# Optimization experiments

Measured on AMD Instinct MI355X. Metric: run time of the kernel, lower is better.

## Reference

```python
import jax, jax.numpy as jnp
import numpy as np

V, E, H, L, T, B, S = 50000, 256, 512, 2, 22, 64, 512
HH = H // 2
START, STOP = T - 2, T - 1  # START_TAG, STOP_TAG appended to tagset


def _lstm_cell(x, h, c, wih, whh, b):
    # PyTorch gate order: i, f, g, o
    g = x @ wih.T + h @ whh.T + b
    i, f, gg, o = jnp.split(g, 4, axis=-1)
    c2 = jax.nn.sigmoid(f) * c + jax.nn.sigmoid(i) * jnp.tanh(gg)
    h2 = jax.nn.sigmoid(o) * jnp.tanh(c2)
    return h2, c2


def _run_dir(xs, ms, h0, c0, wih, whh, b, reverse):
    # xs: [S,B,E], ms: [S,B] bool. Packed-sequence semantics: no state update
    # and zero (pad-value) output at padded steps.
    def step(carry, inp):
        h, c = carry
        xt, mt = inp
        h2, c2 = _lstm_cell(xt, h, c, wih, whh, b)
        m = mt[:, None]
        h = jnp.where(m, h2, h)
        c = jnp.where(m, c2, c)
        return (h, c), jnp.where(m, h, 0.0)
    _, outs = jax.lax.scan(step, (h0, c0), (xs, ms), reverse=reverse)
    return outs


def _forward_feats(sentence, lengths, emb, wih_f, whh_f, b_f, wih_b, whh_b, b_b,
                   h1_0, c1_0, wih_s, whh_s, b_s, h2_0, c2_0, W_tag, b_tag):
    Bq, Sq = sentence.shape
    x = emb[sentence]                                       # [B,S,E]
    ms = (jnp.arange(Sq)[None, :] < lengths[:, None]).T     # [S,B]
    xs = jnp.transpose(x, (1, 0, 2))                        # [S,B,E]
    bc = lambda p: jnp.broadcast_to(p, (Bq, p.shape[-1]))
    out_f = _run_dir(xs, ms, bc(h1_0[0]), bc(c1_0[0]), wih_f, whh_f, b_f, False)
    out_b = _run_dir(xs, ms, bc(h1_0[1]), bc(c1_0[1]), wih_b, whh_b, b_b, True)
    bi = jnp.concatenate([out_f, out_b], axis=-1)           # [S,B,H]

    h0 = jnp.broadcast_to(h2_0, (L, Bq, H))
    c0 = jnp.broadcast_to(c2_0, (L, Bq, H))

    def step(carry, xt):
        h, c = carry
        inp = xt
        hs, cs = [], []
        for l in range(L):  # small fixed layer count
            h2, c2 = _lstm_cell(inp, h[l], c[l], wih_s[l], whh_s[l], b_s[l])
            inp = h2
            hs.append(h2)
            cs.append(c2)
        return (jnp.stack(hs), jnp.stack(cs)), inp

    _, outs = jax.lax.scan(step, (h0, c0), bi)              # [S,B,H]
    feats = jnp.einsum('sbh,th->sbt', outs, W_tag) + b_tag  # [S,B,T]
    return feats, ms


def _viterbi(feats, ms, trans):
    # trans[i, j] = score of transitioning from tag j to tag i
    Tn = trans.shape[0]
    score = feats[0] + trans[:, START][None, :]             # [B,T]

    def vstep(score, inp):
        ft, mt = inp
        cand = score[:, None, :] + trans[None, :, :]        # [B, to, from]
        ns = jnp.max(cand, axis=2) + ft
        bp = jnp.argmax(cand, axis=2)
        m = mt[:, None]
        score = jnp.where(m, ns, score)
        bp = jnp.where(m, bp, jnp.arange(Tn)[None, :])      # identity at pad
        return score, bp

    score, bps = jax.lax.scan(vstep, score, (feats[1:], ms[1:]))
    terminal = score + trans[STOP][None, :]
    best_score = jnp.max(terminal, axis=1)                  # [B]
    best_tag = jnp.argmax(terminal, axis=1)                 # [B]

    def bt(tag, bp):
        nt = jnp.take_along_axis(bp, tag[:, None], axis=1)[:, 0]
        return nt, nt

    _, rest = jax.lax.scan(bt, best_tag, bps, reverse=True)  # [S-1,B]
    tags = jnp.concatenate([rest, best_tag[None, :]], axis=0).T  # [B,S]
    return best_score, tags


def setup_inputs() -> dict:
    key = jax.random.key(0)
    ks = iter(jax.random.split(key, 24))
    sc = 0.08
    n = lambda shape: jax.random.normal(next(ks), shape, dtype=jnp.float32) * sc
    return dict(
        sentence=jax.random.randint(next(ks), (B, S), 0, V),
        lengths=jax.random.randint(next(ks), (B,), 1, S + 1),
        emb=n((V, E)),
        wih_f=n((4 * HH, E)), whh_f=n((4 * HH, HH)), b_f=n((4 * HH,)),
        wih_b=n((4 * HH, E)), whh_b=n((4 * HH, HH)), b_b=n((4 * HH,)),
        h1_0=n((2, 1, HH)), c1_0=n((2, 1, HH)),
        wih_s=n((L, 4 * H, H)), whh_s=n((L, 4 * H, H)), b_s=n((L, 4 * H)),
        h2_0=n((L, 1, H)), c2_0=n((L, 1, H)),
        W_tag=n((T, H)), b_tag=n((T,)),
        trans=n((T, T)),
    )


def reference(sentence, lengths, emb, wih_f, whh_f, b_f, wih_b, whh_b, b_b,
              h1_0, c1_0, wih_s, whh_s, b_s, h2_0, c2_0, W_tag, b_tag, trans):
    feats, ms = _forward_feats(sentence, lengths, emb, wih_f, whh_f, b_f,
                               wih_b, whh_b, b_b, h1_0, c1_0,
                               wih_s, whh_s, b_s, h2_0, c2_0, W_tag, b_tag)
    score, tag_seq = _viterbi(feats, ms, trans)
    return score, tag_seq
```

## Files before the change

### kernel.cpp

```cpp
#include <hip/hip_runtime.h>
#include <cmath>


namespace {
constexpr int SS = 512;
constexpr int BB = 64;
constexpr int EE = 256;
constexpr int HHd = 256;
constexpr int HD = 512;
constexpr int NTAG = 22;
constexpr int TSTART = 20;
constexpr int TSTOP = 21;

constexpr size_t OFF_BI    = 0;
constexpr size_t OFF_H1H   = OFF_BI    + (size_t)SS * HD * BB;
constexpr size_t OFF_XT    = OFF_H1H   + (size_t)(SS + 1) * HD * BB;
constexpr size_t OFF_FEATS = OFF_XT    + (size_t)SS * EE * BB;
constexpr size_t OFF_H0R   = OFF_FEATS + (size_t)SS * NTAG * BB;
constexpr size_t OFF_HF    = OFF_H0R   + 2 * (size_t)HD * BB;
constexpr size_t OFF_HB    = OFF_HF    + 2 * (size_t)HHd * BB;
constexpr size_t OFF_BAR   = OFF_HB    + 2 * (size_t)HHd * BB;
constexpr int BAR_INTS = 1152;

constexpr size_t OFF_C0 = OFF_XT;
constexpr size_t OFF_C1 = OFF_XT + (size_t)HD * BB;
}

__device__ __forceinline__ int cidx(int k, int lane) {
  return ((k >> 2) << 8) + (lane << 2) + (k & 3);
}

__device__ __forceinline__ float4 cload4(const float4* p) {
  float4 r;
  asm volatile("global_load_dwordx4 %0, %1, off sc0 sc1" : "=v"(r) : "v"(p));
  return r;
}
__device__ __forceinline__ void vwait0() {
  asm volatile("s_waitcnt vmcnt(0)" ::: "memory");
}
__device__ __forceinline__ void cstore(float* p, float v) {
  __hip_atomic_store(p, v, __ATOMIC_RELAXED, __HIP_MEMORY_SCOPE_AGENT);
}

template <int NBLK>
__device__ __forceinline__ void gbarC(int* flags, int* release, int bid, int epoch) {
  __syncthreads();
  if (threadIdx.x == 0) {
    __hip_atomic_store(flags + bid, epoch + 1, __ATOMIC_RELAXED, __HIP_MEMORY_SCOPE_AGENT);
  }
  if (bid == 0) {
    if (threadIdx.x < 64) {
      constexpr int PER = NBLK / 64;
      bool ok;
      do {
        ok = true;
#pragma unroll
        for (int i = 0; i < PER; ++i) {
          ok = ok && (__hip_atomic_load(flags + threadIdx.x * PER + i, __ATOMIC_RELAXED,
                                        __HIP_MEMORY_SCOPE_AGENT) > epoch);
        }
      } while (__any(!ok));
      if (threadIdx.x == 0) {
        __hip_atomic_store(release, epoch + 1, __ATOMIC_RELAXED, __HIP_MEMORY_SCOPE_AGENT);
      }
    }
  } else {
    if (threadIdx.x == 0) {
      while (__hip_atomic_load(release, __ATOMIC_RELAXED, __HIP_MEMORY_SCOPE_AGENT) <= epoch) {
        __builtin_amdgcn_s_sleep(1);
      }
    }
  }
  __syncthreads();
}

__device__ __forceinline__ float sigm(float x) { return 1.f / (1.f + expf(-x)); }
__device__ __forceinline__ float comp4(float4 v, int w) {
  return (w == 0) ? v.x : (w == 1) ? v.y : (w == 2) ? v.z : v.w;
}

__global__ __launch_bounds__(256) void k0(const int* __restrict__ sent,
                                          const float* __restrict__ emb,
                                          float* __restrict__ xT) {
  const int t = blockIdx.x;
  const int lane = threadIdx.x & 63;
  const int w = __builtin_amdgcn_readfirstlane(threadIdx.x >> 6);
  __shared__ float tile[64][65];
  __shared__ int rows[64];
  if (threadIdx.x < 64) rows[threadIdx.x] = sent[(size_t)threadIdx.x * SS + t];
  __syncthreads();
  float4* xT4 = (float4*)xT;
  for (int e0 = 0; e0 < EE; e0 += 64) {
    for (int bb = 0; bb < 16; ++bb) {
      int b = bb * 4 + w;
      tile[b][lane] = emb[(size_t)rows[b] * EE + e0 + lane];
    }
    __syncthreads();
    for (int r = 0; r < 4; ++r) {
      int ecl = w * 4 + r;
      int ec = (e0 >> 2) + ecl;
      float4 v = make_float4(tile[lane][ecl * 4 + 0], tile[lane][ecl * 4 + 1],
                             tile[lane][ecl * 4 + 2], tile[lane][ecl * 4 + 3]);
      xT4[((size_t)t * 64 + ec) * 64 + lane] = v;
    }
    __syncthreads();
  }
}

struct K2A {
  const float* xT; float* bi;
  const float* wih_f; const float* whh_f; const float* b_f;
  const float* wih_b; const float* whh_b; const float* b_b;
  const float* h10; const float* c10; const int* lengths;
  float* hf; float* hb;
  int* bar;
};

__global__ __launch_bounds__(512) void k2(K2A a) {
  const int lane = threadIdx.x & 63;
  const int w = __builtin_amdgcn_readfirstlane((int)threadIdx.x >> 6);
  const int d = (int)blockIdx.x >> 7;
  const int lb = (int)blockIdx.x & 127;
  int* flags = a.bar + d * 384;
  int* release = a.bar + d * 384 + 160;
  const int u0 = lb * 2;
  const float* wih = d ? a.wih_b : a.wih_f;
  const float* whh = d ? a.whh_b : a.whh_f;
  const float* bias = d ? a.b_b : a.b_f;
  float* hbuf = d ? a.hb : a.hf;

  __shared__ float lw[8 * 512];
  __shared__ float4 part[8][2][64];

#pragma unroll
  for (int i = 0; i < 2; ++i) {
    int f4 = i * 512 + (int)threadIdx.x;
    int r = f4 >> 7;
    int kk = (f4 & 127) * 4;
    int g = r >> 1, ul = r & 1;
    int grow = g * HHd + u0 + ul;
    float4 v = (kk < 256) ? *(const float4*)(wih + (size_t)grow * 256 + kk)
                          : *(const float4*)(whh + (size_t)grow * 256 + (kk - 256));
    *(float4*)(lw + r * 512 + kk) = v;
  }

  const int len = a.lengths[lane];
  float c_st = 0.f, h_old = 0.f;
  if (w < 2) {
    int u = u0 + w;
    h_old = a.h10[d * 256 + u];
    c_st = a.c10[d * 256 + u];
    cstore(&hbuf[cidx(u, lane)], h_old);
    vwait0();
  }
  int ep = 0;
  gbarC<128>(flags, release, lb, ep); ep++;

  const int ks = w * 64;
  const bool hpart = (w >= 4);
  const float4* lw4 = (const float4*)lw;
  int buf = 0;
  for (int step = 0; step < SS; ++step) {
    const int t = d ? (SS - 1 - step) : step;
    const float* actbase = hpart ? (hbuf + (size_t)buf * (HHd * 64))
                                 : (a.xT + (size_t)t * (EE * 64));
    const int ksl = hpart ? (ks - 256) : ks;
    const float4* p = (const float4*)actbase + (size_t)(ksl >> 2) * 64 + lane;
    float4 va[16];
    if (hpart) {
#pragma unroll
      for (int c = 0; c < 16; ++c) va[c] = cload4(p + (size_t)c * 64);
      vwait0();
    } else {
#pragma unroll
      for (int c = 0; c < 16; ++c) va[c] = p[(size_t)c * 64];
    }
    float acc[8] = {0, 0, 0, 0, 0, 0, 0, 0};
#pragma unroll
    for (int c = 0; c < 16; ++c) {
      float4 h = va[c];
#pragma unroll
      for (int r = 0; r < 8; ++r) {
        float4 wv = lw4[r * 128 + (ks >> 2) + c];
        acc[r] = fmaf(h.x, wv.x, acc[r]);
        acc[r] = fmaf(h.y, wv.y, acc[r]);
        acc[r] = fmaf(h.z, wv.z, acc[r]);
        acc[r] = fmaf(h.w, wv.w, acc[r]);
      }
    }
    part[w][0][lane] = make_float4(acc[0], acc[1], acc[2], acc[3]);
    part[w][1][lane] = make_float4(acc[4], acc[5], acc[6], acc[7]);
    __syncthreads();
    if (w < 2) {
      float qi = 0.f, qf = 0.f, qg = 0.f, qo = 0.f;
#pragma unroll
      for (int wv = 0; wv < 8; ++wv) {
        float4 p0 = part[wv][0][lane], p1 = part[wv][1][lane];
        qi += comp4(p0, w);  qf += comp4(p0, 2 + w);
        qg += comp4(p1, w);  qo += comp4(p1, 2 + w);
      }
      const int u = u0 + w;
      float gi = qi + bias[u];
      float gf = qf + bias[256 + u];
      float gg = qg + bias[512 + u];
      float go = qo + bias[768 + u];
      float i_ = sigm(gi), f_ = sigm(gf), o_ = sigm(go);
      float gn = tanhf(gg);
      float c2 = f_ * c_st + i_ * gn;
      float h2 = o_ * tanhf(c2);
      const bool m = (t < len);
      h2 = m ? h2 : h_old;
      c_st = m ? c2 : c_st;
      h_old = h2;
      cstore(&hbuf[(size_t)(buf ^ 1) * (HHd * 64) + cidx(u, lane)], h2);
      a.bi[(size_t)t * (HD * 64) + cidx(d * 256 + u, lane)] = m ? h2 : 0.f;
      vwait0();
    }
    buf ^= 1;
    gbarC<128>(flags, release, lb, ep); ep++;
  }
}

__global__ __launch_bounds__(512) void k4i(const float* __restrict__ h20,
                                           const float* __restrict__ c20,
                                           float* __restrict__ h0r,
                                           float* __restrict__ h1h,
                                           float* __restrict__ c0,
                                           float* __restrict__ c1) {
  const int layer = blockIdx.x;
  const int u = threadIdx.x;
  const float hv = h20[layer * 512 + u];
  const float cv = c20[layer * 512 + u];
  float* hd = layer ? h1h : h0r;
  float* cd = layer ? c1 : c0;
#pragma unroll 4
  for (int lane = 0; lane < 64; ++lane) {
    hd[cidx(u, lane)] = hv;
    cd[cidx(u, lane)] = cv;
  }
}

struct K4S {
  const float* bi; float* h0r; float* h1h;
  const float* wihs; const float* whhs; const float* bs;
  float* c0; float* c1;
};

__global__ __launch_bounds__(512) void k4s(K4S a, int t) {
  const int layer = (int)blockIdx.x >> 7;
  if (layer == 0) { if (t >= SS) return; } else { if (t < 1) return; }
  const int lane = threadIdx.x & 63;
  const int w = __builtin_amdgcn_readfirstlane((int)threadIdx.x >> 6);
  const int lb = (int)blockIdx.x & 127;
  const int u0 = lb * 4;
  const float* wih = a.wihs + (size_t)layer * (2048 * 512);
  const float* whh = a.whhs + (size_t)layer * (2048 * 512);

  __shared__ float part[4][16][64];

  const int ks = (w & 3) * 128;
  const bool hpart = (w >= 4);
  const float* wsel = hpart ? whh : wih;
  const float* wr[16];
#pragma unroll
  for (int g = 0; g < 4; ++g)
#pragma unroll
    for (int ul = 0; ul < 4; ++ul)
      wr[g * 4 + ul] = wsel + (size_t)(g * HD + u0 + ul) * HD + ks;

  const float* actbase;
  if (layer == 0)
    actbase = hpart ? (a.h0r + (size_t)(t & 1) * (HD * 64))
                    : (a.bi + (size_t)t * (HD * 64));
  else
    actbase = hpart ? (a.h1h + (size_t)(t - 1) * (HD * 64))
                    : (a.h0r + (size_t)(t & 1) * (HD * 64));

  float acc[16] = {0, 0, 0, 0, 0, 0, 0, 0, 0, 0, 0, 0, 0, 0, 0, 0};
  const float4* p = (const float4*)actbase + (size_t)(ks >> 2) * 64 + lane;
#pragma unroll
  for (int gseg = 0; gseg < 2; ++gseg) {
    float4 va[16];
    const float4* pg = p + (size_t)gseg * 16 * 64;
#pragma unroll
    for (int c = 0; c < 16; ++c) va[c] = pg[(size_t)c * 64];
#pragma unroll
    for (int c = 0; c < 16; ++c) {
      float4 h = va[c];
      const int k = (gseg * 16 + c) * 4;
#pragma unroll
      for (int r = 0; r < 16; ++r) {
        float4 wv = *(const float4*)(wr[r] + k);
        acc[r] = fmaf(h.x, wv.x, acc[r]);
        acc[r] = fmaf(h.y, wv.y, acc[r]);
        acc[r] = fmaf(h.z, wv.z, acc[r]);
        acc[r] = fmaf(h.w, wv.w, acc[r]);
      }
    }
  }
  if (w < 4) {
#pragma unroll
    for (int r = 0; r < 16; ++r) part[w][r][lane] = acc[r];
  }
  __syncthreads();
  if (w >= 4) {
#pragma unroll
    for (int r = 0; r < 16; ++r) part[w - 4][r][lane] += acc[r];
  }
  __syncthreads();
  if (w < 4) {
    float q[4];
#pragma unroll
    for (int g = 0; g < 4; ++g) {
      float s = 0.f;
#pragma unroll
      for (int sl = 0; sl < 4; ++sl) s += part[sl][g * 4 + w][lane];
      q[g] = s;
    }
    const int u = u0 + w;
    const float* bsl = a.bs + (size_t)layer * 2048;
    float* cst = layer ? a.c1 : a.c0;
    float c_st = cst[cidx(u, lane)];
    float gi = q[0] + bsl[u];
    float gf = q[1] + bsl[512 + u];
    float gg = q[2] + bsl[1024 + u];
    float go = q[3] + bsl[1536 + u];
    float i_ = sigm(gi), f_ = sigm(gf), o_ = sigm(go);
    float gn = tanhf(gg);
    float c2 = f_ * c_st + i_ * gn;
    float h2 = o_ * tanhf(c2);
    cst[cidx(u, lane)] = c2;
    if (layer == 0)
      a.h0r[(size_t)((t + 1) & 1) * (HD * 64) + cidx(u, lane)] = h2;
    else
      a.h1h[(size_t)t * (HD * 64) + cidx(u, lane)] = h2;
  }
}

__global__ __launch_bounds__(256) void k4b(const float* __restrict__ h1h,
                                           const float* __restrict__ Wtag,
                                           const float* __restrict__ btag,
                                           float* __restrict__ feats) {
  const int t = blockIdx.x;
  const int lane = threadIdx.x & 63;
  const int w = __builtin_amdgcn_readfirstlane(threadIdx.x >> 6);
  const int j0 = w * 6;
  const float4* p = (const float4*)(h1h + (size_t)(t + 1) * (HD * 64)) + lane;
  const float* r[6];
  float acc[6];
#pragma unroll
  for (int jj = 0; jj < 6; ++jj) {
    int j = j0 + jj; if (j > 21) j = 21;
    r[jj] = Wtag + (size_t)j * HD;
    acc[jj] = btag[j];
  }
#pragma unroll 2
  for (int c = 0; c < 128; ++c) {
    float4 h = p[(size_t)c * 64];
    int k = c * 4;
#pragma unroll
    for (int jj = 0; jj < 6; ++jj) {
      acc[jj] = fmaf(h.x, r[jj][k], acc[jj]);
      acc[jj] = fmaf(h.y, r[jj][k + 1], acc[jj]);
      acc[jj] = fmaf(h.z, r[jj][k + 2], acc[jj]);
      acc[jj] = fmaf(h.w, r[jj][k + 3], acc[jj]);
    }
  }
#pragma unroll
  for (int jj = 0; jj < 6; ++jj) {
    int j = j0 + jj;
    if (j < NTAG) feats[((size_t)t * NTAG + j) * 64 + lane] = acc[jj];
  }
}

__global__ __launch_bounds__(64) void k5(const float* __restrict__ feats,
                                         const float* __restrict__ trans,
                                         const int* __restrict__ lengths,
                                         float* __restrict__ out) {
  const int b = blockIdx.x;
  const int j = threadIdx.x;
  __shared__ float tr[NTAG * NTAG];
  __shared__ float sc[NTAG];
  __shared__ float term[NTAG];
  __shared__ unsigned char bp[SS - 1][NTAG];
  for (int i = j; i < NTAG * NTAG; i += 64) tr[i] = trans[i];
  const int len = lengths[b];
  float score = 0.f;
  __syncthreads();
  if (j < NTAG) {
    score = feats[(size_t)j * 64 + b] + tr[j * NTAG + TSTART];
    sc[j] = score;
  }
  __syncthreads();
  for (int t = 1; t < len; ++t) {
    float best = -3.4e38f; int bi_ = 0;
    if (j < NTAG) {
#pragma unroll
      for (int i = 0; i < NTAG; ++i) {
        float c = sc[i] + tr[j * NTAG + i];
        if (c > best) { best = c; bi_ = i; }
      }
      score = best + feats[((size_t)t * NTAG + j) * 64 + b];
      bp[t - 1][j] = (unsigned char)bi_;
    }
    __syncthreads();
    if (j < NTAG) sc[j] = score;
    __syncthreads();
  }
  if (j < NTAG) term[j] = score + tr[TSTOP * NTAG + j];
  __syncthreads();
  if (j == 0) {
    float bs = term[0]; int bt = 0;
    for (int i = 1; i < NTAG; ++i) if (term[i] > bs) { bs = term[i]; bt = i; }
    out[b] = bs;
    int tag = bt;
    for (int t = SS - 1; t >= 1; --t) {
      out[64 + (size_t)b * SS + t] = (float)tag;
      if (t < len) tag = bp[t - 1][tag];
    }
    out[64 + (size_t)b * SS + 0] = (float)tag;
  }
}

extern "C" void kernel_launch(void* const* d_in, const int* in_sizes, int n_in,
                              void* d_out, int out_size, void* d_ws, size_t ws_size,
                              hipStream_t stream) {
  const int* sentence = (const int*)d_in[0];
  const int* lengths  = (const int*)d_in[1];
  const float* emb    = (const float*)d_in[2];
  const float* wih_f  = (const float*)d_in[3];
  const float* whh_f  = (const float*)d_in[4];
  const float* b_f    = (const float*)d_in[5];
  const float* wih_b  = (const float*)d_in[6];
  const float* whh_b  = (const float*)d_in[7];
  const float* b_b    = (const float*)d_in[8];
  const float* h10    = (const float*)d_in[9];
  const float* c10    = (const float*)d_in[10];
  const float* wihs   = (const float*)d_in[11];
  const float* whhs   = (const float*)d_in[12];
  const float* bs     = (const float*)d_in[13];
  const float* h20    = (const float*)d_in[14];
  const float* c20    = (const float*)d_in[15];
  const float* Wtag   = (const float*)d_in[16];
  const float* btag   = (const float*)d_in[17];
  const float* trans  = (const float*)d_in[18];
  float* ws = (float*)d_ws;
  float* out = (float*)d_out;
  int* barbase = (int*)(ws + OFF_BAR);

  hipMemsetAsync((void*)barbase, 0, BAR_INTS * sizeof(int), stream);

  k0<<<dim3(SS), dim3(256), 0, stream>>>(sentence, emb, ws + OFF_XT);

  K2A a2{ws + OFF_XT, ws + OFF_BI, wih_f, whh_f, b_f, wih_b, whh_b, b_b,
         h10, c10, lengths,
         ws + OFF_HF, ws + OFF_HB,
         barbase};
  k2<<<dim3(256), dim3(512), 0, stream>>>(a2);

  k4i<<<dim3(2), dim3(512), 0, stream>>>(h20, c20, ws + OFF_H0R, ws + OFF_H1H,
                                         ws + OFF_C0, ws + OFF_C1);
  K4S a4{ws + OFF_BI, ws + OFF_H0R, ws + OFF_H1H, wihs, whhs, bs,
         ws + OFF_C0, ws + OFF_C1};
  for (int t = 0; t <= SS; ++t) {
    k4s<<<dim3(256), dim3(512), 0, stream>>>(a4, t);
  }

  k4b<<<dim3(SS), dim3(256), 0, stream>>>(ws + OFF_H1H, Wtag, btag, ws + OFF_FEATS);
  k5<<<dim3(BB), dim3(64), 0, stream>>>(ws + OFF_FEATS, trans, lengths, out);
}
```

Measured before the change: 12.66 ms.

## Fuse stacked-LSTM timestep launches into one persistent cooperative kernel

Replaces 513 per-timestep launches of the stacked LSTM kernel with a single cooperative kernel that loops over time and uses grid.sync between steps. The cell state now stays in registers across steps instead of round-tripping through global memory. This removes per-launch overhead, at the cost of a grid-wide barrier each step and the requirement that all 256 blocks be co-resident.

Measured after the change: 36.73 ms. 190% more time.

```diff
diff --git a/kernel.cpp b/kernel.cpp
--- a/kernel.cpp
+++ b/kernel.cpp
@@ -1,6 +1,9 @@
 #include <hip/hip_runtime.h>
+#include <hip/hip_cooperative_groups.h>
 #include <cmath>
 
+
+namespace cg = cooperative_groups;
 
 namespace {
 constexpr int SS = 512;
@@ -21,9 +24,6 @@
 constexpr size_t OFF_HB    = OFF_HF    + 2 * (size_t)HHd * BB;
 constexpr size_t OFF_BAR   = OFF_HB    + 2 * (size_t)HHd * BB;
 constexpr int BAR_INTS = 1152;
-
-constexpr size_t OFF_C0 = OFF_XT;
-constexpr size_t OFF_C1 = OFF_XT + (size_t)HD * BB;
 }
 
 __device__ __forceinline__ int cidx(int k, int lane) {
@@ -222,35 +222,29 @@
 }
 
 __global__ __launch_bounds__(512) void k4i(const float* __restrict__ h20,
-                                           const float* __restrict__ c20,
                                            float* __restrict__ h0r,
-                                           float* __restrict__ h1h,
-                                           float* __restrict__ c0,
-                                           float* __restrict__ c1) {
+                                           float* __restrict__ h1h) {
   const int layer = blockIdx.x;
   const int u = threadIdx.x;
   const float hv = h20[layer * 512 + u];
-  const float cv = c20[layer * 512 + u];
   float* hd = layer ? h1h : h0r;
-  float* cd = layer ? c1 : c0;
 #pragma unroll 4
   for (int lane = 0; lane < 64; ++lane) {
     hd[cidx(u, lane)] = hv;
-    cd[cidx(u, lane)] = cv;
   }
 }
 
 struct K4S {
   const float* bi; float* h0r; float* h1h;
   const float* wihs; const float* whhs; const float* bs;
-  float* c0; float* c1;
+  const float* h20; const float* c20;
 };
 
-__global__ __launch_bounds__(512) void k4s(K4S a, int t) {
-  const int layer = (int)blockIdx.x >> 7;
-  if (layer == 0) { if (t >= SS) return; } else { if (t < 1) return; }
+__global__ __launch_bounds__(512) void k4c(K4S a) {
+  cg::grid_group grid = cg::this_grid();
   const int lane = threadIdx.x & 63;
   const int w = __builtin_amdgcn_readfirstlane((int)threadIdx.x >> 6);
+  const int layer = (int)blockIdx.x >> 7;
   const int lb = (int)blockIdx.x & 127;
   const int u0 = lb * 4;
   const float* wih = a.wihs + (size_t)layer * (2048 * 512);
@@ -268,72 +262,78 @@
     for (int ul = 0; ul < 4; ++ul)
       wr[g * 4 + ul] = wsel + (size_t)(g * HD + u0 + ul) * HD + ks;
 
-  const float* actbase;
-  if (layer == 0)
-    actbase = hpart ? (a.h0r + (size_t)(t & 1) * (HD * 64))
-                    : (a.bi + (size_t)t * (HD * 64));
-  else
-    actbase = hpart ? (a.h1h + (size_t)(t - 1) * (HD * 64))
-                    : (a.h0r + (size_t)(t & 1) * (HD * 64));
-
-  float acc[16] = {0, 0, 0, 0, 0, 0, 0, 0, 0, 0, 0, 0, 0, 0, 0, 0};
-  const float4* p = (const float4*)actbase + (size_t)(ks >> 2) * 64 + lane;
-#pragma unroll
-  for (int gseg = 0; gseg < 2; ++gseg) {
-    float4 va[16];
-    const float4* pg = p + (size_t)gseg * 16 * 64;
-#pragma unroll
-    for (int c = 0; c < 16; ++c) va[c] = pg[(size_t)c * 64];
-#pragma unroll
-    for (int c = 0; c < 16; ++c) {
-      float4 h = va[c];
-      const int k = (gseg * 16 + c) * 4;
-#pragma unroll
-      for (int r = 0; r < 16; ++r) {
-        float4 wv = *(const float4*)(wr[r] + k);
-        acc[r] = fmaf(h.x, wv.x, acc[r]);
-        acc[r] = fmaf(h.y, wv.y, acc[r]);
-        acc[r] = fmaf(h.z, wv.z, acc[r]);
-        acc[r] = fmaf(h.w, wv.w, acc[r]);
-      }
-    }
-  }
-  if (w < 4) {
-#pragma unroll
-    for (int r = 0; r < 16; ++r) part[w][r][lane] = acc[r];
-  }
-  __syncthreads();
-  if (w >= 4) {
-#pragma unroll
-    for (int r = 0; r < 16; ++r) part[w - 4][r][lane] += acc[r];
-  }
-  __syncthreads();
-  if (w < 4) {
-    float q[4];
-#pragma unroll
-    for (int g = 0; g < 4; ++g) {
-      float s = 0.f;
-#pragma unroll
-      for (int sl = 0; sl < 4; ++sl) s += part[sl][g * 4 + w][lane];
-      q[g] = s;
-    }
-    const int u = u0 + w;
-    const float* bsl = a.bs + (size_t)layer * 2048;
-    float* cst = layer ? a.c1 : a.c0;
-    float c_st = cst[cidx(u, lane)];
-    float gi = q[0] + bsl[u];
-    float gf = q[1] + bsl[512 + u];
-    float gg = q[2] + bsl[1024 + u];
-    float go = q[3] + bsl[1536 + u];
-    float i_ = sigm(gi), f_ = sigm(gf), o_ = sigm(go);
-    float gn = tanhf(gg);
-    float c2 = f_ * c_st + i_ * gn;
-    float h2 = o_ * tanhf(c2);
-    cst[cidx(u, lane)] = c2;
-    if (layer == 0)
-      a.h0r[(size_t)((t + 1) & 1) * (HD * 64) + cidx(u, lane)] = h2;
-    else
-      a.h1h[(size_t)t * (HD * 64) + cidx(u, lane)] = h2;
+  float c_st = 0.f;
+  if (w < 4) c_st = a.c20[layer * 512 + u0 + w];
+  const float* bsl = a.bs + (size_t)layer * 2048;
+
+  for (int t = 0; t <= SS; ++t) {
+    const bool active = (layer == 0) ? (t < SS) : (t >= 1);
+    float acc[16] = {0, 0, 0, 0, 0, 0, 0, 0, 0, 0, 0, 0, 0, 0, 0, 0};
+    if (active) {
+      const float* actbase;
+      if (layer == 0)
+        actbase = hpart ? (a.h0r + (size_t)(t & 1) * (HD * 64))
+                        : (a.bi + (size_t)t * (HD * 64));
+      else
+        actbase = hpart ? (a.h1h + (size_t)(t - 1) * (HD * 64))
+                        : (a.h0r + (size_t)(t & 1) * (HD * 64));
+      const float4* p = (const float4*)actbase + (size_t)(ks >> 2) * 64 + lane;
+#pragma unroll
+      for (int gseg = 0; gseg < 2; ++gseg) {
+        float4 va[16];
+        const float4* pg = p + (size_t)gseg * 16 * 64;
+#pragma unroll
+        for (int c = 0; c < 16; ++c) va[c] = pg[(size_t)c * 64];
+#pragma unroll
+        for (int c = 0; c < 16; ++c) {
+          float4 h = va[c];
+          const int k = (gseg * 16 + c) * 4;
+#pragma unroll
+          for (int r = 0; r < 16; ++r) {
+            float4 wv = *(const float4*)(wr[r] + k);
+            acc[r] = fmaf(h.x, wv.x, acc[r]);
+            acc[r] = fmaf(h.y, wv.y, acc[r]);
+            acc[r] = fmaf(h.z, wv.z, acc[r]);
+            acc[r] = fmaf(h.w, wv.w, acc[r]);
+          }
+        }
+      }
+    }
+    if (w < 4) {
+#pragma unroll
+      for (int r = 0; r < 16; ++r) part[w][r][lane] = acc[r];
+    }
+    __syncthreads();
+    if (w >= 4) {
+#pragma unroll
+      for (int r = 0; r < 16; ++r) part[w - 4][r][lane] += acc[r];
+    }
+    __syncthreads();
+    if (active && w < 4) {
+      float q[4];
+#pragma unroll
+      for (int g = 0; g < 4; ++g) {
+        float s = 0.f;
+#pragma unroll
+        for (int sl = 0; sl < 4; ++sl) s += part[sl][g * 4 + w][lane];
+        q[g] = s;
+      }
+      const int u = u0 + w;
+      float gi = q[0] + bsl[u];
+      float gf = q[1] + bsl[512 + u];
+      float gg = q[2] + bsl[1024 + u];
+      float go = q[3] + bsl[1536 + u];
+      float i_ = sigm(gi), f_ = sigm(gf), o_ = sigm(go);
+      float gn = tanhf(gg);
+      float c2 = f_ * c_st + i_ * gn;
+      float h2 = o_ * tanhf(c2);
+      c_st = c2;
+      if (layer == 0)
+        a.h0r[(size_t)((t + 1) & 1) * (HD * 64) + cidx(u, lane)] = h2;
+      else
+        a.h1h[(size_t)t * (HD * 64) + cidx(u, lane)] = h2;
+    }
+    grid.sync();
   }
 }
 
@@ -458,13 +458,10 @@
          barbase};
   k2<<<dim3(256), dim3(512), 0, stream>>>(a2);
 
-  k4i<<<dim3(2), dim3(512), 0, stream>>>(h20, c20, ws + OFF_H0R, ws + OFF_H1H,
-                                         ws + OFF_C0, ws + OFF_C1);
-  K4S a4{ws + OFF_BI, ws + OFF_H0R, ws + OFF_H1H, wihs, whhs, bs,
-         ws + OFF_C0, ws + OFF_C1};
-  for (int t = 0; t <= SS; ++t) {
-    k4s<<<dim3(256), dim3(512), 0, stream>>>(a4, t);
-  }
+  k4i<<<dim3(2), dim3(512), 0, stream>>>(h20, ws + OFF_H0R, ws + OFF_H1H);
+  K4S a4{ws + OFF_BI, ws + OFF_H0R, ws + OFF_H1H, wihs, whhs, bs, h20, c20};
+  void* kargs[] = { (void*)&a4 };
+  hipLaunchCooperativeKernel((void*)k4c, dim3(256), dim3(512), kargs, 0, stream);
 
   k4b<<<dim3(SS), dim3(256), 0, stream>>>(ws + OFF_H1H, Wtag, btag, ws + OFF_FEATS);
   k5<<<dim3(BB), dim3(64), 0, stream>>>(ws + OFF_FEATS, trans, lengths, out);
```
